# Performance work log

Measured on AMD Instinct MI355X. Metric: run time of the kernel, lower is better.

## Reference

```python
import jax, jax.numpy as jnp
from jax import lax
import numpy as np

V, PV, DV, DIRV = 50000, 50, 50, 4
ED, POSD, DEPD, DIRD = 300, 4, 5, 1
H, NREL = 60, 5
IN = ED + POSD + DEPD + DIRD  # 310
B, P, L = 1024, 16, 8


def setup_inputs() -> dict:
    key = jax.random.key(0)
    ks = jax.random.split(key, 24)
    inp = {
        'word_idx': jax.random.randint(ks[0], (B, P, L), 0, V),
        'pos_idx': jax.random.randint(ks[1], (B, P, L), 0, PV),
        'dep_idx': jax.random.randint(ks[2], (B, P, L), 0, DV),
        'dir_idx': jax.random.randint(ks[3], (B, P, L), 0, DIRV),
        'lengths': 1 + jax.random.randint(ks[4], (B, P), 0, L),  # 1..L valid edges
        'counts': jnp.ones((B, P), jnp.float32),
        'pair_idx': jax.random.randint(ks[5], (B, 2), 0, V),
        # learned parameters
        'word_emb': jax.random.normal(ks[6], (V, ED), jnp.float32) * 0.02,
        'pos_emb': jax.random.normal(ks[7], (PV, POSD), jnp.float32) * 0.02,
        'dep_emb': jax.random.normal(ks[8], (DV, DEPD), jnp.float32) * 0.02,
        'dir_emb': jax.random.normal(ks[9], (DIRV, DIRD), jnp.float32) * 0.02,
        'Wih0': jax.random.normal(ks[10], (4 * H, IN), jnp.float32) * 0.05,
        'Whh0': jax.random.normal(ks[11], (4 * H, H), jnp.float32) * 0.05,
        'bih0': jnp.zeros((4 * H,), jnp.float32),
        'bhh0': jnp.zeros((4 * H,), jnp.float32),
        'Wih1': jax.random.normal(ks[12], (4 * H, H), jnp.float32) * 0.05,
        'Whh1': jax.random.normal(ks[13], (4 * H, H), jnp.float32) * 0.05,
        'bih1': jnp.zeros((4 * H,), jnp.float32),
        'bhh1': jnp.zeros((4 * H,), jnp.float32),
        'W': jax.random.normal(ks[14], (NREL, ED + H + ED), jnp.float32) * 0.02,
        'b': jnp.zeros((NREL,), jnp.float32),
    }
    return inp


def _lstm_layer(x, Wih, Whh, bih, bhh):
    # x: [L, N, D] -> outputs [L, N, H]  (torch gate order: i, f, g, o)
    n = x.shape[1]
    h0 = jnp.zeros((n, Whh.shape[1]), x.dtype)
    bias = bih + bhh

    def step(carry, xt):
        h, c = carry
        g = xt @ Wih.T + h @ Whh.T + bias
        i, f, gg, o = jnp.split(g, 4, axis=-1)
        c = jax.nn.sigmoid(f) * c + jax.nn.sigmoid(i) * jnp.tanh(gg)
        h = jax.nn.sigmoid(o) * jnp.tanh(c)
        return (h, c), h

    _, hs = lax.scan(step, (h0, h0), x)
    return hs


def reference(word_idx, pos_idx, dep_idx, dir_idx, lengths, counts, pair_idx,
              word_emb, pos_emb, dep_emb, dir_emb,
              Wih0, Whh0, bih0, bhh0, Wih1, Whh1, bih1, bhh1, W, b):
    b_, p_, l_ = word_idx.shape
    n = b_ * p_
    # per-edge embedding gather + concat -> [B, P, L, 310]
    feats = jnp.concatenate([
        word_emb[word_idx], pos_emb[pos_idx], dep_emb[dep_idx], dir_emb[dir_idx]
    ], axis=-1)
    x = feats.reshape(n, l_, -1).transpose(1, 0, 2)  # [L, N, 310]
    h1 = _lstm_layer(x, Wih0, Whh0, bih0, bhh0)       # [L, N, H]
    h2 = _lstm_layer(h1, Wih1, Whh1, bih1, bhh1)      # [L, N, H]
    # last valid timestep per ragged path (causal scan => safe gather)
    lens = lengths.reshape(n)
    last = h2[lens - 1, jnp.arange(n)]                # [N, H]
    last = last.reshape(b_, p_, -1)
    # count-weighted mean over paths per pair
    path_emb = (last * counts[..., None]).sum(1) / counts.sum(1, keepdims=True)
    xw = word_emb[pair_idx[:, 0]]
    yw = word_emb[pair_idx[:, 1]]
    feat = jnp.concatenate([xw, path_emb, yw], axis=-1)  # [B, 660]
    logits = feat @ W.T + b
    return jax.nn.softmax(logits, axis=-1)
```

## Files before the change

kernel.cpp:

```cpp
#include <hip/hip_runtime.h>
#include <math.h>

#define ED 300
#define Hh 60
#define G4 240
#define NRELc 5
#define Bc 1024
#define Pc 16
#define Lc 8
#define Nc (Bc*Pc)
#define VOC 50000
#define TROW 256
#define POS0 50000
#define DEP0 50050
#define DIR0 50100
#define NTROWS 50104

typedef __attribute__((ext_vector_type(8))) short short8v;
typedef __attribute__((ext_vector_type(4))) short short4v;
typedef __attribute__((ext_vector_type(4))) unsigned short ushort4v;
typedef __attribute__((ext_vector_type(4))) float f32x4;
typedef unsigned short u16;

__device__ __forceinline__ float sigf(float x){ return 1.f/(1.f+__expf(-x)); }
__device__ __forceinline__ float tanhfast(float x){
    x = fminf(fmaxf(x,-15.f),15.f);
    float e = __expf(-2.f*x);
    return (1.f-e)/(1.f+e);
}
__device__ __forceinline__ u16 f2b(float f){
    union{float f; unsigned u;} v; v.f=f;
    unsigned r = v.u + 0x7fffu + ((v.u>>16)&1u);
    return (u16)(r>>16);
}
__device__ __forceinline__ float b2f(u16 b){ return __uint_as_float(((unsigned)b)<<16); }
__device__ __forceinline__ float blo(unsigned d){ return __uint_as_float(d<<16); }
__device__ __forceinline__ float bhi(unsigned d){ return __uint_as_float(d & 0xffff0000u); }
__device__ __forceinline__ int origrow(int j){ return (j&3)*60 + (j>>2); }

__global__ __launch_bounds__(256) void prep_kernel(
    const float* __restrict__ Wih0, const float* __restrict__ Whh0,
    const float* __restrict__ Wih1, const float* __restrict__ Whh1,
    const float* __restrict__ bih0, const float* __restrict__ bhh0,
    const float* __restrict__ bih1, const float* __restrict__ bhh1,
    const float* __restrict__ pemb, const float* __restrict__ demb,
    const float* __restrict__ remb,
    u16* __restrict__ Aswz0, u16* __restrict__ A0P, u16* __restrict__ A1P,
    u16* __restrict__ tab)
{
    const int i0 = blockIdx.x*256 + threadIdx.x;
    const int stride = gridDim.x*256;
    for (int idx=i0; idx<15*10*64*8; idx+=stride){
        int e = idx&7, l = (idx>>3)&63, mk = idx>>9;
        int m = mk/10, ks = mk - m*10;
        int j = origrow(m*16 + (l&15));
        int k = ks*32 + ((e>>2)<<4) + ((l>>4)<<2) + (e&3);
        float v = 0.f;
        if (k < 310)      v = Wih0[j*310 + k];
        else if (k==310)  v = bih0[j] + bhh0[j];
        Aswz0[idx] = f2b(v);
    }
    for (int idx=i0; idx<15*2*64*8; idx+=stride){
        int e = idx&7, l = (idx>>3)&63, mk = idx>>9;
        int m = mk>>1, ks = mk&1;
        int j = origrow(m*16 + (l&15));
        int k = ks*32 + ((e>>2)<<4) + ((l>>4)<<2) + (e&3);
        A0P[idx] = f2b(k<60 ? Whh0[j*60+k] : 0.f);
    }
    for (int idx=i0; idx<15*4*64*8; idx+=stride){
        int e = idx&7, l = (idx>>3)&63, mk = idx>>9;
        int m = mk>>2, ks = mk&3;
        int j = origrow(m*16 + (l&15));
        int k = ks*32 + ((e>>2)<<4) + ((l>>4)<<2) + (e&3);
        float v = 0.f;
        if (k < 60)                  v = Wih1[j*60 + k];
        else if (k == 60)            v = bih1[j] + bhh1[j];
        else if (k >= 64 && k < 124) v = Whh1[j*60 + (k-64)];
        A1P[idx] = f2b(v);
    }
    for (int idx=i0; idx<50*240; idx+=stride){
        int p = idx/240, j = idx - p*240;
        int oj = origrow(j);
        float v = 0.f;
        for (int q=0;q<4;q++) v += Wih0[oj*310 + 300+q]*pemb[p*4+q];
        tab[(size_t)(POS0+p)*TROW + j] = f2b(v);
        float w = 0.f;
        for (int q=0;q<5;q++) w += Wih0[oj*310 + 304+q]*demb[p*5+q];
        tab[(size_t)(DEP0+p)*TROW + j] = f2b(w);
    }
    for (int idx=i0; idx<4*240; idx+=stride){
        int d = idx/240, j = idx - d*240;
        int oj = origrow(j);
        float v = remb[d]*Wih0[oj*310 + 309] + bih0[oj] + bhh0[oj];
        tab[(size_t)(DIR0+d)*TROW + j] = f2b(v);
    }
}

__global__ __launch_bounds__(256,2) void wxa_kernel(
    const float* __restrict__ wemb, const u16* __restrict__ Aswz,
    u16* __restrict__ tab)
{
    const int tid = threadIdx.x;
    const int l  = tid & 63;
    const int wv = __builtin_amdgcn_readfirstlane(tid>>6);
    const int r0 = blockIdx.x*128;
    const int row0 = wv*32 + (l&15);
    const int v0 = r0 + row0, v1 = v0 + 16;
    const int v0c = v0 < VOC ? v0 : VOC-1;
    const int v1c = v1 < VOC ? v1 : VOC-1;
    const float* b0p = wemb + (size_t)v0c*300;
    const float* b1p = wemb + (size_t)v1c*300;

    f32x4 acc[15][2];
#pragma unroll
    for (int m=0;m<15;m++){
        acc[m][0] = f32x4{0.f,0.f,0.f,0.f};
        acc[m][1] = f32x4{0.f,0.f,0.f,0.f};
    }
    const float4 z4 = {0.f,0.f,0.f,0.f};
#pragma unroll
    for (int ks=0; ks<10; ++ks){
        const int k0 = ks*32 + ((l>>4)<<2);
        const int k1 = k0 + 16;
        float4 a0 = (k0<300) ? *(const float4*)(b0p+k0) : z4;
        float4 a1 = (k1<300) ? *(const float4*)(b0p+k1) : z4;
        float4 c0 = (k0<300) ? *(const float4*)(b1p+k0) : z4;
        float4 c1 = (k1<300) ? *(const float4*)(b1p+k1) : z4;
        short8v bf0 = {(short)f2b(a0.x),(short)f2b(a0.y),(short)f2b(a0.z),(short)f2b(a0.w),
                       (short)f2b(a1.x),(short)f2b(a1.y),(short)f2b(a1.z),(short)f2b(a1.w)};
        short8v bf1 = {(short)f2b(c0.x),(short)f2b(c0.y),(short)f2b(c0.z),(short)f2b(c0.w),
                       (short)f2b(c1.x),(short)f2b(c1.y),(short)f2b(c1.z),(short)f2b(c1.w)};
#pragma unroll
        for (int m=0;m<15;m++){
            short8v a = *(const short8v*)(Aswz + (size_t)(((m*10+ks)<<6) + l)*8);
            acc[m][0] = __builtin_amdgcn_mfma_f32_16x16x32_bf16(a, bf0, acc[m][0], 0,0,0);
            acc[m][1] = __builtin_amdgcn_mfma_f32_16x16x32_bf16(a, bf1, acc[m][1], 0,0,0);
        }
    }
#pragma unroll
    for (int m=0;m<15;m++){
        const int j = m*16 + ((l>>4)<<2);
        ushort4v s0, s1;
#pragma unroll
        for (int i=0;i<4;i++){ s0[i]=f2b(acc[m][0][i]); s1[i]=f2b(acc[m][1][i]); }
        if (v0 < VOC) *(ushort4v*)(tab + (size_t)v0*TROW + j) = s0;
        if (v1 < VOC) *(ushort4v*)(tab + (size_t)v1*TROW + j) = s1;
    }
}

__global__ __launch_bounds__(256,1) void recf_kernel(
    const int* __restrict__ widx, const int* __restrict__ pidx,
    const int* __restrict__ didx, const int* __restrict__ ridx,
    const u16* __restrict__ tab,
    const u16* __restrict__ A0P, const u16* __restrict__ A1P,
    const int* __restrict__ lens, float* __restrict__ lastT)
{
    __shared__ u16 ldsA0[15*2*64*8];
    __shared__ u16 ldsA1[15*4*64*8];
    __shared__ u16 hb1[64][68];
    __shared__ u16 hb2[64][68];
    __shared__ __align__(16) unsigned offsL[8][64][4];

    const int tid = threadIdx.x;
    const int l   = tid & 63;
    const int w   = __builtin_amdgcn_readfirstlane(tid>>6);
    const int nn  = l & 15;
    const int gq  = l >> 4;
    const int jo  = gq << 2;
    const int n0  = blockIdx.x*64;

    {
        const uint4* s0 = (const uint4*)A0P;
        const uint4* s1 = (const uint4*)A1P;
        uint4* d0 = (uint4*)ldsA0;
        uint4* d1 = (uint4*)ldsA1;
        for (int i=tid; i<15*2*64; i+=256) d0[i] = s0[i];
        for (int i=tid; i<15*4*64; i+=256) d1[i] = s1[i];
    }
    for (int i=tid; i<512; i+=256){
        int t = i & 7, s = i >> 3;
        int n = n0 + s;
        offsL[t][s][0] = (unsigned)widx[n*Lc+t] << 9;
        offsL[t][s][1] = (unsigned)(POS0 + pidx[n*Lc+t]) << 9;
        offsL[t][s][2] = (unsigned)(DEP0 + didx[n*Lc+t]) << 9;
        offsL[t][s][3] = (unsigned)(DIR0 + ridx[n*Lc+t]) << 9;
    }
    for (int i=tid; i<64*68; i+=256){ ((u16*)hb1)[i]=0; ((u16*)hb2)[i]=0; }
    __syncthreads();
    if (tid < 64) hb1[tid][60] = 0x3F80;
    float c1[4][4], c2[4][4];
#pragma unroll
    for (int a=0;a<4;a++)
#pragma unroll
        for (int b=0;b<4;b++){ c1[a][b]=0.f; c2[a][b]=0.f; }
    int ln[4];
#pragma unroll
    for (int nt=0;nt<4;nt++) ln[nt] = lens[n0 + nt*16 + nn];
    __syncthreads();

    const char* tabb = (const char*)tab;

    for (int t=0;t<Lc;t++){
        f32x4 acc[4][4];
        uint4 of[4];
#pragma unroll
        for (int nt=0;nt<4;nt++) of[nt] = *(const uint4*)&offsL[t][nt*16+nn][0];
#pragma unroll
        for (int ml=0;ml<4;ml++){
            const int m = w*4 + ml;
            if (m < 15){
                const int jb = (m*16 + jo)*2;
#pragma unroll
                for (int nt=0;nt<4;nt++){
                    uint2 ga = *(const uint2*)(tabb + of[nt].x + jb);
                    uint2 gb = *(const uint2*)(tabb + of[nt].y + jb);
                    uint2 gc = *(const uint2*)(tabb + of[nt].z + jb);
                    uint2 gd = *(const uint2*)(tabb + of[nt].w + jb);
                    f32x4 v;
                    v[0] = blo(ga.x)+blo(gb.x)+blo(gc.x)+blo(gd.x);
                    v[1] = bhi(ga.x)+bhi(gb.x)+bhi(gc.x)+bhi(gd.x);
                    v[2] = blo(ga.y)+blo(gb.y)+blo(gc.y)+blo(gd.y);
                    v[3] = bhi(ga.y)+bhi(gb.y)+bhi(gc.y)+bhi(gd.y);
                    acc[ml][nt] = v;
                }
            }
        }
#pragma unroll
        for (int ks=0;ks<2;ks++){
            short8v bfr[4];
#pragma unroll
            for (int nt=0;nt<4;nt++){
                const u16* row = &hb1[nt*16+nn][0];
                short4v lo = *(const short4v*)(row + ks*32 + jo);
                short4v hi = *(const short4v*)(row + ks*32 + jo + 16);
                bfr[nt] = short8v{lo[0],lo[1],lo[2],lo[3],hi[0],hi[1],hi[2],hi[3]};
            }
#pragma unroll
            for (int ml=0;ml<4;ml++){
                const int m = w*4 + ml;
                if (m < 15){
                    short8v a = *(const short8v*)(ldsA0 + (size_t)(((m*2+ks)<<6)+l)*8);
#pragma unroll
                    for (int nt=0;nt<4;nt++)
                        acc[ml][nt] = __builtin_amdgcn_mfma_f32_16x16x32_bf16(a, bfr[nt], acc[ml][nt], 0,0,0);
                }
            }
        }
        __syncthreads();
#pragma unroll
        for (int ml=0;ml<4;ml++){
            const int m = w*4 + ml;
            if (m < 15){
                const int u = m*4 + gq;
#pragma unroll
                for (int nt=0;nt<4;nt++){
                    float gi = sigf(acc[ml][nt][0]);
                    float gf = sigf(acc[ml][nt][1]);
                    float gg = tanhfast(acc[ml][nt][2]);
                    float go = sigf(acc[ml][nt][3]);
                    float cc = gf*c1[ml][nt] + gi*gg;
                    c1[ml][nt] = cc;
                    hb1[nt*16+nn][u] = f2b(go*tanhfast(cc));
                }
            }
        }
        __syncthreads();
#pragma unroll
        for (int ml=0;ml<4;ml++)
#pragma unroll
            for (int nt=0;nt<4;nt++) acc[ml][nt] = f32x4{0.f,0.f,0.f,0.f};
#pragma unroll
        for (int ks=0;ks<4;ks++){
            short8v bfr[4];
#pragma unroll
            for (int nt=0;nt<4;nt++){
                const u16* row = (ks<2) ? &hb1[nt*16+nn][0] : &hb2[nt*16+nn][0];
                const int kb = (ks&1)*32 + jo;
                short4v lo = *(const short4v*)(row + kb);
                short4v hi = *(const short4v*)(row + kb + 16);
                bfr[nt] = short8v{lo[0],lo[1],lo[2],lo[3],hi[0],hi[1],hi[2],hi[3]};
            }
#pragma unroll
            for (int ml=0;ml<4;ml++){
                const int m = w*4 + ml;
                if (m < 15){
                    short8v a = *(const short8v*)(ldsA1 + (size_t)(((m*4+ks)<<6)+l)*8);
#pragma unroll
                    for (int nt=0;nt<4;nt++)
                        acc[ml][nt] = __builtin_amdgcn_mfma_f32_16x16x32_bf16(a, bfr[nt], acc[ml][nt], 0,0,0);
                }
            }
        }
        __syncthreads();
#pragma unroll
        for (int ml=0;ml<4;ml++){
            const int m = w*4 + ml;
            if (m < 15){
                const int u = m*4 + gq;
#pragma unroll
                for (int nt=0;nt<4;nt++){
                    float gi = sigf(acc[ml][nt][0]);
                    float gf = sigf(acc[ml][nt][1]);
                    float gg = tanhfast(acc[ml][nt][2]);
                    float go = sigf(acc[ml][nt][3]);
                    float cc = gf*c2[ml][nt] + gi*gg;
                    c2[ml][nt] = cc;
                    float h = go*tanhfast(cc);
                    hb2[nt*16+nn][u] = f2b(h);
                    if (t == ln[nt]-1) lastT[(size_t)u*Nc + n0 + nt*16 + nn] = h;
                }
            }
        }
        __syncthreads();
    }
}

__global__ __launch_bounds__(320) void final_kernel(
    const float* __restrict__ lastT, const float* __restrict__ counts,
    const int* __restrict__ pair, const float* __restrict__ wemb,
    const float* __restrict__ W, const float* __restrict__ bvec,
    float* __restrict__ out)
{
    __shared__ float path[Hh];
    __shared__ float red[NRELc];
    const int b = blockIdx.x;
    const int tid = threadIdx.x;

    if (tid < Hh){
        float sum=0.f, cs=0.f;
        for (int p=0;p<Pc;p++){
            float cnt = counts[b*Pc+p];
            sum += lastT[(size_t)tid*Nc + b*Pc+p]*cnt;
            cs  += cnt;
        }
        path[tid] = sum/cs;
    }
    __syncthreads();

    const int rrel = tid>>6;
    const int lane = tid&63;
    const int xi = pair[b*2+0], yi = pair[b*2+1];
    const float* Wr = W + rrel*(2*ED+Hh);
    float acc=0.f;
    for (int d=lane; d<ED; d+=64) acc += wemb[xi*ED+d]*Wr[d];
    for (int k=lane; k<Hh; k+=64) acc += path[k]*Wr[ED+k];
    for (int d=lane; d<ED; d+=64) acc += wemb[yi*ED+d]*Wr[ED+Hh+d];
    for (int off=32; off>0; off>>=1) acc += __shfl_down(acc, off);
    if (lane==0) red[rrel] = acc + bvec[rrel];
    __syncthreads();

    if (tid==0){
        float m=red[0];
        for (int i=1;i<NRELc;i++) m=fmaxf(m,red[i]);
        float e[NRELc]; float sum=0.f;
        for (int i=0;i<NRELc;i++){ e[i]=__expf(red[i]-m); sum+=e[i]; }
        float inv=1.f/sum;
        for (int i=0;i<NRELc;i++) out[b*NRELc+i]=e[i]*inv;
    }
}

extern "C" void kernel_launch(void* const* d_in, const int* in_sizes, int n_in,
                              void* d_out, int out_size, void* d_ws, size_t ws_size,
                              hipStream_t stream)
{
    const int*   word_idx = (const int*)d_in[0];
    const int*   pos_idx  = (const int*)d_in[1];
    const int*   dep_idx  = (const int*)d_in[2];
    const int*   dir_idx  = (const int*)d_in[3];
    const int*   lengths  = (const int*)d_in[4];
    const float* counts   = (const float*)d_in[5];
    const int*   pair_idx = (const int*)d_in[6];
    const float* word_emb = (const float*)d_in[7];
    const float* pos_emb  = (const float*)d_in[8];
    const float* dep_emb  = (const float*)d_in[9];
    const float* dir_emb  = (const float*)d_in[10];
    const float* Wih0     = (const float*)d_in[11];
    const float* Whh0     = (const float*)d_in[12];
    const float* bih0     = (const float*)d_in[13];
    const float* bhh0     = (const float*)d_in[14];
    const float* Wih1     = (const float*)d_in[15];
    const float* Whh1     = (const float*)d_in[16];
    const float* bih1     = (const float*)d_in[17];
    const float* bhh1     = (const float*)d_in[18];
    const float* W        = (const float*)d_in[19];
    const float* bvec     = (const float*)d_in[20];
    float* out = (float*)d_out;

    float* p = (float*)d_ws;
    float* lastT = p; p += (size_t)Nc*Hh;
    u16* q = (u16*)p;
    u16* Aswz0 = q; q += 15*10*64*8;
    u16* A0P   = q; q += 15*2*64*8;
    u16* A1P   = q; q += 15*4*64*8;
    u16* tab   = q; q += (size_t)NTROWS*TROW;

    prep_kernel<<<256,256,0,stream>>>(Wih0,Whh0,Wih1,Whh1,bih0,bhh0,bih1,bhh1,
                                      pos_emb,dep_emb,dir_emb,
                                      Aswz0,A0P,A1P,tab);
    wxa_kernel<<<(VOC+127)/128,256,0,stream>>>(word_emb,Aswz0,tab);
    recf_kernel<<<Nc/64,256,0,stream>>>(word_idx,pos_idx,dep_idx,dir_idx,
                                        tab,A0P,A1P,lengths,lastT);
    final_kernel<<<Bc,320,0,stream>>>(lastT,counts,pair_idx,word_emb,W,bvec,out);
}
```

Baseline: 305.2 us.

## Split gather-add into separate kernel and widen recurrence blocks to 12 waves

Moves the per-timestep four-table gather and sum into its own kernel, which writes precomputed layer-0 input gates to a bf16 staging buffer in MFMA fragment order. The recurrence kernel now runs 768 threads (12 waves), each owning one 16-sequence tile and 5 gate rows, with the layer-0 recurrent weights held in registers rather than LDS. The lastT output layout becomes sequence-major. This aims to take the latency-bound random gathers off the serial recurrence and add more waves per block. In exchange it adds an extra global round trip through the staging buffer, a second rounding of the summed gates to bf16, and a kernel launch.

```diff
diff --git a/kernel.cpp b/kernel.cpp
--- a/kernel.cpp
+++ b/kernel.cpp
@@ -15,6 +15,7 @@
 #define DEP0 50050
 #define DIR0 50100
 #define NTROWS 50104
+#define NTILES 8192
 
 typedef __attribute__((ext_vector_type(8))) short short8v;
 typedef __attribute__((ext_vector_type(4))) short short4v;
@@ -148,170 +149,147 @@
     }
 }
 
-__global__ __launch_bounds__(256,1) void recf_kernel(
+__global__ __launch_bounds__(256,4) void gadd_kernel(
     const int* __restrict__ widx, const int* __restrict__ pidx,
     const int* __restrict__ didx, const int* __restrict__ ridx,
-    const u16* __restrict__ tab,
+    const u16* __restrict__ tab, u16* __restrict__ ginF)
+{
+    const int tid = threadIdx.x;
+    const int l  = tid & 63;
+    const int wv = tid >> 6;
+    const int s  = blockIdx.x*4 + wv;
+    const int t  = s >> 10;
+    const int n  = ((s & 1023)<<4) + (l&15);
+    const int w  = widx[n*Lc+t];
+    const int p  = pidx[n*Lc+t];
+    const int d  = didx[n*Lc+t];
+    const int dd = ridx[n*Lc+t];
+    const u16* rw = tab + (size_t)w*TROW;
+    const u16* rp = tab + (size_t)(POS0+p)*TROW;
+    const u16* rd = tab + (size_t)(DEP0+d)*TROW;
+    const u16* rr = tab + (size_t)(DIR0+dd)*TROW;
+    const int j0 = (l>>4)<<2;
+
+#pragma unroll
+    for (int m=0;m<15;m++){
+        const int j = m*16 + j0;
+        uint2 aw = *(const uint2*)(rw + j);
+        uint2 ap = *(const uint2*)(rp + j);
+        uint2 ad = *(const uint2*)(rd + j);
+        uint2 ar = *(const uint2*)(rr + j);
+        ushort4v o;
+        o[0] = f2b(blo(aw.x)+blo(ap.x)+blo(ad.x)+blo(ar.x));
+        o[1] = f2b(bhi(aw.x)+bhi(ap.x)+bhi(ad.x)+bhi(ar.x));
+        o[2] = f2b(blo(aw.y)+blo(ap.y)+blo(ad.y)+blo(ar.y));
+        o[3] = f2b(bhi(aw.y)+bhi(ap.y)+bhi(ad.y)+bhi(ar.y));
+        *(ushort4v*)(ginF + (((size_t)s*15+m)<<8) + (l<<2)) = o;
+    }
+}
+
+__global__ __launch_bounds__(768,3) void recf_kernel(
+    const u16* __restrict__ ginF,
     const u16* __restrict__ A0P, const u16* __restrict__ A1P,
     const int* __restrict__ lens, float* __restrict__ lastT)
 {
-    __shared__ u16 ldsA0[15*2*64*8];
     __shared__ u16 ldsA1[15*4*64*8];
     __shared__ u16 hb1[64][68];
     __shared__ u16 hb2[64][68];
-    __shared__ __align__(16) unsigned offsL[8][64][4];
 
     const int tid = threadIdx.x;
     const int l   = tid & 63;
     const int w   = __builtin_amdgcn_readfirstlane(tid>>6);
+    const int mg  = w >> 2;
+    const int nt  = w & 3;
     const int nn  = l & 15;
     const int gq  = l >> 4;
     const int jo  = gq << 2;
     const int n0  = blockIdx.x*64;
+    const int seq = nt*16 + nn;
 
     {
-        const uint4* s0 = (const uint4*)A0P;
         const uint4* s1 = (const uint4*)A1P;
-        uint4* d0 = (uint4*)ldsA0;
         uint4* d1 = (uint4*)ldsA1;
-        for (int i=tid; i<15*2*64; i+=256) d0[i] = s0[i];
-        for (int i=tid; i<15*4*64; i+=256) d1[i] = s1[i];
-    }
-    for (int i=tid; i<512; i+=256){
-        int t = i & 7, s = i >> 3;
-        int n = n0 + s;
-        offsL[t][s][0] = (unsigned)widx[n*Lc+t] << 9;
-        offsL[t][s][1] = (unsigned)(POS0 + pidx[n*Lc+t]) << 9;
-        offsL[t][s][2] = (unsigned)(DEP0 + didx[n*Lc+t]) << 9;
-        offsL[t][s][3] = (unsigned)(DIR0 + ridx[n*Lc+t]) << 9;
-    }
-    for (int i=tid; i<64*68; i+=256){ ((u16*)hb1)[i]=0; ((u16*)hb2)[i]=0; }
+        for (int i=tid; i<15*4*64; i+=768) d1[i] = s1[i];
+    }
+    short8v a0r[5][2];
+#pragma unroll
+    for (int ml=0; ml<5; ml++){
+        const int m = mg*5 + ml;
+#pragma unroll
+        for (int ks=0; ks<2; ks++)
+            a0r[ml][ks] = *(const short8v*)(A0P + (size_t)(((m*2+ks)<<6)+l)*8);
+    }
+    for (int i=tid; i<64*68; i+=768){ ((u16*)hb1)[i]=0; ((u16*)hb2)[i]=0; }
     __syncthreads();
     if (tid < 64) hb1[tid][60] = 0x3F80;
-    float c1[4][4], c2[4][4];
-#pragma unroll
-    for (int a=0;a<4;a++)
-#pragma unroll
-        for (int b=0;b<4;b++){ c1[a][b]=0.f; c2[a][b]=0.f; }
-    int ln[4];
-#pragma unroll
-    for (int nt=0;nt<4;nt++) ln[nt] = lens[n0 + nt*16 + nn];
+    float c1[5], c2[5];
+#pragma unroll
+    for (int i=0;i<5;i++){ c1[i]=0.f; c2[i]=0.f; }
+    const int ln = lens[n0 + seq];
     __syncthreads();
 
-    const char* tabb = (const char*)tab;
-
     for (int t=0;t<Lc;t++){
-        f32x4 acc[4][4];
-        uint4 of[4];
-#pragma unroll
-        for (int nt=0;nt<4;nt++) of[nt] = *(const uint4*)&offsL[t][nt*16+nn][0];
-#pragma unroll
-        for (int ml=0;ml<4;ml++){
-            const int m = w*4 + ml;
-            if (m < 15){
-                const int jb = (m*16 + jo)*2;
-#pragma unroll
-                for (int nt=0;nt<4;nt++){
-                    uint2 ga = *(const uint2*)(tabb + of[nt].x + jb);
-                    uint2 gb = *(const uint2*)(tabb + of[nt].y + jb);
-                    uint2 gc = *(const uint2*)(tabb + of[nt].z + jb);
-                    uint2 gd = *(const uint2*)(tabb + of[nt].w + jb);
-                    f32x4 v;
-                    v[0] = blo(ga.x)+blo(gb.x)+blo(gc.x)+blo(gd.x);
-                    v[1] = bhi(ga.x)+bhi(gb.x)+bhi(gc.x)+bhi(gd.x);
-                    v[2] = blo(ga.y)+blo(gb.y)+blo(gc.y)+blo(gd.y);
-                    v[3] = bhi(ga.y)+bhi(gb.y)+bhi(gc.y)+bhi(gd.y);
-                    acc[ml][nt] = v;
-                }
+        const size_t s = (size_t)t*1024 + blockIdx.x*4 + nt;
+        f32x4 acc[5];
+#pragma unroll
+        for (int ml=0;ml<5;ml++){
+            const int m = mg*5 + ml;
+            ushort4v g4 = *(const ushort4v*)(ginF + (((size_t)s*15+m)<<8) + (l<<2));
+            acc[ml] = f32x4{ b2f(g4[0]), b2f(g4[1]), b2f(g4[2]), b2f(g4[3]) };
+        }
+#pragma unroll
+        for (int ks=0;ks<2;ks++){
+            const u16* row = &hb1[seq][0];
+            short4v lo = *(const short4v*)(row + ks*32 + jo);
+            short4v hi = *(const short4v*)(row + ks*32 + jo + 16);
+            short8v b = {lo[0],lo[1],lo[2],lo[3],hi[0],hi[1],hi[2],hi[3]};
+#pragma unroll
+            for (int ml=0;ml<5;ml++)
+                acc[ml] = __builtin_amdgcn_mfma_f32_16x16x32_bf16(a0r[ml][ks], b, acc[ml], 0,0,0);
+        }
+        __syncthreads();
+#pragma unroll
+        for (int ml=0;ml<5;ml++){
+            const int u = (mg*5+ml)*4 + gq;
+            float gi = sigf(acc[ml][0]);
+            float gf = sigf(acc[ml][1]);
+            float gg = tanhfast(acc[ml][2]);
+            float go = sigf(acc[ml][3]);
+            float cc = gf*c1[ml] + gi*gg;
+            c1[ml] = cc;
+            hb1[seq][u] = f2b(go*tanhfast(cc));
+        }
+        __syncthreads();
+#pragma unroll
+        for (int ml=0;ml<5;ml++) acc[ml] = f32x4{0.f,0.f,0.f,0.f};
+#pragma unroll
+        for (int ks=0;ks<4;ks++){
+            const u16* row = (ks<2) ? &hb1[seq][0] : &hb2[seq][0];
+            const int kb = (ks&1)*32 + jo;
+            short4v lo = *(const short4v*)(row + kb);
+            short4v hi = *(const short4v*)(row + kb + 16);
+            short8v b = {lo[0],lo[1],lo[2],lo[3],hi[0],hi[1],hi[2],hi[3]};
+#pragma unroll
+            for (int ml=0;ml<5;ml++){
+                const int m = mg*5 + ml;
+                short8v a = *(const short8v*)(ldsA1 + (size_t)(((m*4+ks)<<6)+l)*8);
+                acc[ml] = __builtin_amdgcn_mfma_f32_16x16x32_bf16(a, b, acc[ml], 0,0,0);
             }
         }
-#pragma unroll
-        for (int ks=0;ks<2;ks++){
-            short8v bfr[4];
-#pragma unroll
-            for (int nt=0;nt<4;nt++){
-                const u16* row = &hb1[nt*16+nn][0];
-                short4v lo = *(const short4v*)(row + ks*32 + jo);
-                short4v hi = *(const short4v*)(row + ks*32 + jo + 16);
-                bfr[nt] = short8v{lo[0],lo[1],lo[2],lo[3],hi[0],hi[1],hi[2],hi[3]};
-            }
-#pragma unroll
-            for (int ml=0;ml<4;ml++){
-                const int m = w*4 + ml;
-                if (m < 15){
-                    short8v a = *(const short8v*)(ldsA0 + (size_t)(((m*2+ks)<<6)+l)*8);
-#pragma unroll
-                    for (int nt=0;nt<4;nt++)
-                        acc[ml][nt] = __builtin_amdgcn_mfma_f32_16x16x32_bf16(a, bfr[nt], acc[ml][nt], 0,0,0);
-                }
-            }
-        }
         __syncthreads();
 #pragma unroll
-        for (int ml=0;ml<4;ml++){
-            const int m = w*4 + ml;
-            if (m < 15){
-                const int u = m*4 + gq;
-#pragma unroll
-                for (int nt=0;nt<4;nt++){
-                    float gi = sigf(acc[ml][nt][0]);
-                    float gf = sigf(acc[ml][nt][1]);
-                    float gg = tanhfast(acc[ml][nt][2]);
-                    float go = sigf(acc[ml][nt][3]);
-                    float cc = gf*c1[ml][nt] + gi*gg;
-                    c1[ml][nt] = cc;
-                    hb1[nt*16+nn][u] = f2b(go*tanhfast(cc));
-                }
-            }
-        }
-        __syncthreads();
-#pragma unroll
-        for (int ml=0;ml<4;ml++)
-#pragma unroll
-            for (int nt=0;nt<4;nt++) acc[ml][nt] = f32x4{0.f,0.f,0.f,0.f};
-#pragma unroll
-        for (int ks=0;ks<4;ks++){
-            short8v bfr[4];
-#pragma unroll
-            for (int nt=0;nt<4;nt++){
-                const u16* row = (ks<2) ? &hb1[nt*16+nn][0] : &hb2[nt*16+nn][0];
-                const int kb = (ks&1)*32 + jo;
-                short4v lo = *(const short4v*)(row + kb);
-                short4v hi = *(const short4v*)(row + kb + 16);
-                bfr[nt] = short8v{lo[0],lo[1],lo[2],lo[3],hi[0],hi[1],hi[2],hi[3]};
-            }
-#pragma unroll
-            for (int ml=0;ml<4;ml++){
-                const int m = w*4 + ml;
-                if (m < 15){
-                    short8v a = *(const short8v*)(ldsA1 + (size_t)(((m*4+ks)<<6)+l)*8);
-#pragma unroll
-                    for (int nt=0;nt<4;nt++)
-                        acc[ml][nt] = __builtin_amdgcn_mfma_f32_16x16x32_bf16(a, bfr[nt], acc[ml][nt], 0,0,0);
-                }
-            }
-        }
-        __syncthreads();
-#pragma unroll
-        for (int ml=0;ml<4;ml++){
-            const int m = w*4 + ml;
-            if (m < 15){
-                const int u = m*4 + gq;
-#pragma unroll
-                for (int nt=0;nt<4;nt++){
-                    float gi = sigf(acc[ml][nt][0]);
-                    float gf = sigf(acc[ml][nt][1]);
-                    float gg = tanhfast(acc[ml][nt][2]);
-                    float go = sigf(acc[ml][nt][3]);
-                    float cc = gf*c2[ml][nt] + gi*gg;
-                    c2[ml][nt] = cc;
-                    float h = go*tanhfast(cc);
-                    hb2[nt*16+nn][u] = f2b(h);
-                    if (t == ln[nt]-1) lastT[(size_t)u*Nc + n0 + nt*16 + nn] = h;
-                }
-            }
-        }
-        __syncthreads();
+        for (int ml=0;ml<5;ml++){
+            const int u = (mg*5+ml)*4 + gq;
+            float gi = sigf(acc[ml][0]);
+            float gf = sigf(acc[ml][1]);
+            float gg = tanhfast(acc[ml][2]);
+            float go = sigf(acc[ml][3]);
+            float cc = gf*c2[ml] + gi*gg;
+            c2[ml] = cc;
+            float h = go*tanhfast(cc);
+            hb2[seq][u] = f2b(h);
+            if (t == ln-1) lastT[(size_t)(n0+seq)*64 + u] = h;
+        }
     }
 }
 
@@ -330,7 +308,7 @@
         float sum=0.f, cs=0.f;
         for (int p=0;p<Pc;p++){
             float cnt = counts[b*Pc+p];
-            sum += lastT[(size_t)tid*Nc + b*Pc+p]*cnt;
+            sum += lastT[(size_t)(b*Pc+p)*64 + tid]*cnt;
             cs  += cnt;
         }
         path[tid] = sum/cs;
@@ -387,18 +365,19 @@
     float* out = (float*)d_out;
 
     float* p = (float*)d_ws;
-    float* lastT = p; p += (size_t)Nc*Hh;
+    float* lastT = p; p += (size_t)Nc*64;
     u16* q = (u16*)p;
     u16* Aswz0 = q; q += 15*10*64*8;
     u16* A0P   = q; q += 15*2*64*8;
     u16* A1P   = q; q += 15*4*64*8;
     u16* tab   = q; q += (size_t)NTROWS*TROW;
+    u16* ginF  = q; q += (size_t)NTILES*15*256;
 
     prep_kernel<<<256,256,0,stream>>>(Wih0,Whh0,Wih1,Whh1,bih0,bhh0,bih1,bhh1,
                                       pos_emb,dep_emb,dir_emb,
                                       Aswz0,A0P,A1P,tab);
     wxa_kernel<<<(VOC+127)/128,256,0,stream>>>(word_emb,Aswz0,tab);
-    recf_kernel<<<Nc/64,256,0,stream>>>(word_idx,pos_idx,dep_idx,dir_idx,
-                                        tab,A0P,A1P,lengths,lastT);
+    gadd_kernel<<<NTILES/4,256,0,stream>>>(word_idx,pos_idx,dep_idx,dir_idx,tab,ginF);
+    recf_kernel<<<Nc/64,768,0,stream>>>(ginF,A0P,A1P,lengths,lastT);
     final_kernel<<<Bc,320,0,stream>>>(lastT,counts,pair_idx,word_emb,W,bvec,out);
 }
```

Result: faster. 293.2 us (-3.9%).
